# Performance work log

Measured on AMD Instinct MI355X. Metric: run time of the kernel, lower is better.

Reference implementation:

```python
import jax, jax.numpy as jnp
import numpy as np

B, S, DIM, NQ, NKV = 2, 2048, 4096, 32, 8
HD = DIM // NQ  # 128


def _rope(t, fc):
    # t: [B,S,H,D]; fc: [S,D/2,2] = (cos,sin). Complex multiply on (even,odd) pairs.
    b, s, h, d = t.shape
    tp = t.astype(jnp.float32).reshape(b, s, h, d // 2, 2)
    c = fc[None, :, None, :, 0]
    sn = fc[None, :, None, :, 1]
    x0, x1 = tp[..., 0], tp[..., 1]
    rot = jnp.stack([x0 * c - x1 * sn, x0 * sn + x1 * c], axis=-1)
    return rot.reshape(b, s, h, d).astype(t.dtype)


def setup_inputs() -> dict:
    key = jax.random.key(0)
    ks = jax.random.split(key, 5)
    x = jax.random.normal(ks[0], (B, S, DIM), jnp.float32)
    wq = jax.random.normal(ks[1], (DIM, NQ * HD), jnp.float32) * 0.02
    wk = jax.random.normal(ks[2], (DIM, NKV * HD), jnp.float32) * 0.02
    wv = jax.random.normal(ks[3], (DIM, NKV * HD), jnp.float32) * 0.02
    wo = jax.random.normal(ks[4], (NQ * HD, DIM), jnp.float32) * 0.02
    # Llama RoPE frequencies for positions [0, S)
    inv_freq = 1.0 / (10000.0 ** (jnp.arange(0, HD, 2, dtype=jnp.float32) / HD))
    ang = jnp.arange(S, dtype=jnp.float32)[:, None] * inv_freq[None, :]  # [S, HD/2]
    freqs_cis = jnp.stack([jnp.cos(ang), jnp.sin(ang)], axis=-1)  # [S, HD/2, 2]
    cache_key = jnp.zeros((B, S, NKV, HD), jnp.float32)
    cache_value = jnp.zeros((B, S, NKV, HD), jnp.float32)
    return {"x": x, "start_pos": 0, "freqs_cis": freqs_cis, "wq": wq, "wk": wk,
            "wv": wv, "wo": wo, "cache_key": cache_key, "cache_value": cache_value}


def reference(x, start_pos, freqs_cis, wq, wk, wv, wo, cache_key, cache_value):
    b, s, dim = x.shape
    nkv, hd = cache_key.shape[2], cache_key.shape[3]
    nq = wq.shape[1] // hd
    n_rep = nq // nkv
    xq = (x @ wq).reshape(b, s, nq, hd)
    xk = (x @ wk).reshape(b, s, nkv, hd)
    xv = (x @ wv).reshape(b, s, nkv, hd)
    xq = _rope(xq, freqs_cis)
    xk = _rope(xk, freqs_cis)
    # KV-cache write then read of the valid prefix
    ck = jax.lax.dynamic_update_slice(cache_key, xk, (0, start_pos, 0, 0))
    cv = jax.lax.dynamic_update_slice(cache_value, xv, (0, start_pos, 0, 0))
    kv_len = start_pos + s
    k = ck[:, :kv_len]
    v = cv[:, :kv_len]
    # GQA: repeat_interleave kv heads to match q heads (as original materializes)
    keys = jnp.repeat(k, n_rep, axis=2)    # [B,K,NQ,HD]
    values = jnp.repeat(v, n_rep, axis=2)
    scale = 1.0 / jnp.sqrt(jnp.float32(hd))
    scores = jnp.einsum('bqhd,bkhd->bhqk', xq, keys) * scale  # [B,H,S,K]
    attn = jax.nn.softmax(scores, axis=-1)  # NOTE: no causal mask, as in source
    out = jnp.einsum('bhqk,bkhd->bqhd', attn, values).reshape(b, s, nq * hd)
    return out @ wo
```

## Files before the change

### kernel.cpp

```cpp
#include <hip/hip_runtime.h>
#include <stdint.h>


typedef __attribute__((ext_vector_type(8))) short short8;
typedef __attribute__((ext_vector_type(4))) float f32x4;
typedef __attribute__((ext_vector_type(16))) float f32x16;

#define DEVFN static __device__ __forceinline__

DEVFN ushort f2bf(float f) {
  uint32_t u = __builtin_bit_cast(uint32_t, f);
  u += 0x7fffu + ((u >> 16) & 1);
  return (ushort)(u >> 16);
}

DEVFN void gll16(const void* g, void* l) {
  __builtin_amdgcn_global_load_lds(
      (const __attribute__((address_space(1))) void*)g,
      (__attribute__((address_space(3))) void*)l, 16, 0, 0);
}

DEVFN float xhalf_max(float v) { return fmaxf(v, __shfl_xor(v, 32)); }
DEVFN float xhalf_add(float v) { return v + __shfl_xor(v, 32); }

#if __has_builtin(__builtin_amdgcn_exp2f)
DEVFN float ex2(float x) { return __builtin_amdgcn_exp2f(x); }
#else
DEVFN float ex2(float x) {
  float r;
  asm("v_exp_f32 %0, %1" : "=v"(r) : "v"(x));
  return r;
}
#endif

DEVFN uint32_t cvtpk(float a, float b) {
  uint32_t r;
  asm("v_cvt_pk_bf16_f32 %0, %1, %2" : "=v"(r) : "v"(a), "v"(b));
  return r;
}

DEVFN float vmax16(const f32x16& v) {
  float a0 = fmaxf(fmaxf(v[0], v[1]), v[2]);
  float a1 = fmaxf(fmaxf(v[3], v[4]), v[5]);
  float a2 = fmaxf(fmaxf(v[6], v[7]), v[8]);
  float a3 = fmaxf(fmaxf(v[9], v[10]), v[11]);
  float a4 = fmaxf(fmaxf(v[12], v[13]), v[14]);
  float b0 = fmaxf(fmaxf(a0, a1), a2);
  float b1 = fmaxf(fmaxf(a3, a4), v[15]);
  return fmaxf(b0, b1);
}
DEVFN float vsum16(const f32x16& v) {
  float s0 = (v[0] + v[1]) + (v[2] + v[3]);
  float s1 = (v[4] + v[5]) + (v[6] + v[7]);
  float s2 = (v[8] + v[9]) + (v[10] + v[11]);
  float s3 = (v[12] + v[13]) + (v[14] + v[15]);
  return (s0 + s1) + (s2 + s3);
}

DEVFN short8 mk_frag(uint32_t w0, uint32_t w1, uint32_t w2, uint32_t w3, int hi) {
  uint32_t x0 = __shfl_xor(w0, 32);
  uint32_t x1 = __shfl_xor(w1, 32);
  uint32_t x2 = __shfl_xor(w2, 32);
  uint32_t x3 = __shfl_xor(w3, 32);
  uint4 u;
  u.x = hi ? x2 : w0;
  u.y = hi ? x3 : w1;
  u.z = hi ? w2 : x0;
  u.w = hi ? w3 : x1;
  return __builtin_bit_cast(short8, u);
}

#define VMW(N) asm volatile("s_waitcnt vmcnt(" #N ")" ::: "memory")

__global__ __launch_bounds__(256) void k_cvt(const float* __restrict__ src,
                                             ushort* __restrict__ dst, int n8) {
  int i = blockIdx.x * 256 + threadIdx.x;
  if (i >= n8) return;
  const float4* s4 = (const float4*)src + (size_t)i * 2;
  float4 a = s4[0], b = s4[1];
  uint4 o;
  o.x = (uint32_t)f2bf(a.x) | ((uint32_t)f2bf(a.y) << 16);
  o.y = (uint32_t)f2bf(a.z) | ((uint32_t)f2bf(a.w) << 16);
  o.z = (uint32_t)f2bf(b.x) | ((uint32_t)f2bf(b.y) << 16);
  o.w = (uint32_t)f2bf(b.z) | ((uint32_t)f2bf(b.w) << 16);
  ((uint4*)dst)[i] = o;
}

__global__ __launch_bounds__(256) void k_tr(const float* __restrict__ src,
                                            ushort* __restrict__ dst, int R, int C) {
  __shared__ float tile[64][65];
  const int c0 = blockIdx.x * 64, r0 = blockIdx.y * 64;
  const int t = threadIdx.x, rr = t >> 6, cc = t & 63;
#pragma unroll
  for (int i = 0; i < 16; ++i)
    tile[rr + i * 4][cc] = src[(size_t)(r0 + rr + i * 4) * C + c0 + cc];
  __syncthreads();
#pragma unroll
  for (int i = 0; i < 16; ++i)
    dst[(size_t)(c0 + rr + i * 4) * R + r0 + cc] = f2bf(tile[cc][rr + i * 4]);
}

template <int MODE>
__global__ __launch_bounds__(512, 2) void k_gemm8(
    const ushort* __restrict__ A, const ushort* __restrict__ Bp,
    const float* __restrict__ fcis, ushort* __restrict__ oQ,
    ushort* __restrict__ oK, ushort* __restrict__ oV, float* __restrict__ oC) {
  constexpr int K = 4096;
  constexpr int BN = MODE ? 256 : 192;
  constexpr int WN = BN / 4;
  constexpr int NF = WN / 16;
  constexpr int NBX = MODE ? 16 : 32;
  constexpr int ABUF = 16384;
  constexpr int BBUF = BN * 64;
  constexpr int NT = K / 32;

  __shared__ char smem[4 * ABUF + 4 * BBUF];
  char* AsL = smem;
  char* BsL = smem + 4 * ABUF;

  constexpr int nwg = NBX * 16;
  const int bid = blockIdx.x;
  const int wg = (bid & 7) * (nwg >> 3) + (bid >> 3);
  const int nb = wg % NBX, mb = wg / NBX;
  const int m0 = mb * 256, n0 = nb * BN;

  const int tid = threadIdx.x;
  const int w = tid >> 6, lane = tid & 63;
  const int gg = lane >> 4, rr = lane & 15;
  const int wm = w >> 2, wn = w & 3;

  const int l8 = lane >> 3, s7 = lane & 7;
  const int Ra0 = w * 8 + l8, Ra1 = 64 + Ra0;
  const int ea0 = s7 ^ (Ra0 & 7), ea1 = s7 ^ (Ra1 & 7);
  const ushort* agp0 = A + (size_t)(m0 + 2 * Ra0 + (ea0 >> 2)) * K + (ea0 & 3) * 8;
  const ushort* agp1 = A + (size_t)(m0 + 2 * Ra1 + (ea1 >> 2)) * K + (ea1 & 3) * 8;
  char* lda0 = AsL + w * 1024;
  char* lda1 = AsL + 8192 + w * 1024;

  const int Rb0 = w * 8 + l8;
  const int eb0 = s7 ^ (Rb0 & 7);
  const ushort* bgp0 = Bp + (size_t)(n0 + 2 * Rb0 + (eb0 >> 2)) * K + (eb0 & 3) * 8;
  char* ldb0 = BsL + w * 1024;
  const int Rb1 = MODE ? (64 + w * 8 + l8) : (64 + w * 4 + l8);
  const int eb1 = s7 ^ (Rb1 & 7);
  const ushort* bgp1 = Bp + (size_t)(n0 + 2 * Rb1 + (eb1 >> 2)) * K + (eb1 & 3) * 8;
  char* ldb1 = BsL + 8192 + (MODE ? w * 1024 : w * 512);

  auto STAGE_A = [&](int t) {
    const int bo = t & 3;
    const size_t ko = (size_t)t * 32;
    gll16(agp0 + ko, lda0 + bo * ABUF);
    gll16(agp1 + ko, lda1 + bo * ABUF);
  };
  auto STAGE_B = [&](int t) {
    const int bo = t & 3;
    const size_t ko = (size_t)t * 32;
    gll16(bgp0 + ko, ldb0 + bo * BBUF);
    if constexpr (MODE) {
      gll16(bgp1 + ko, ldb1 + bo * BBUF);
    } else {
      if (lane < 32) gll16(bgp1 + ko, ldb1 + bo * BBUF);
    }
  };

  int aoff[8], boff[NF];
#pragma unroll
  for (int mf = 0; mf < 8; ++mf) {
    const int m = wm * 128 + mf * 16 + rr;
    aoff[mf] = (m >> 1) * 128 + (((((m & 1) << 2) | gg) ^ ((m >> 1) & 7)) << 4);
  }
#pragma unroll
  for (int nf = 0; nf < NF; ++nf) {
    const int n = wn * WN + nf * 16 + rr;
    boff[nf] = (n >> 1) * 128 + (((((n & 1) << 2) | gg) ^ ((n >> 1) & 7)) << 4);
  }

  f32x4 acc[8][NF] = {};
  short8 X0[4], X1[4], Y0[4], Y1[4];
  short8 Bc0[NF], Bc1[NF];

  auto RD_A = [&](int tt, short8* d, int h) {
    const char* Ab = AsL + (tt & 3) * ABUF;
#pragma unroll
    for (int i = 0; i < 4; ++i) d[i] = *(const short8*)(Ab + aoff[h * 4 + i]);
  };
  auto RD_B = [&](int tt, short8* d) {
    const char* Bb = BsL + (tt & 3) * BBUF;
#pragma unroll
    for (int nf = 0; nf < NF; ++nf) d[nf] = *(const short8*)(Bb + boff[nf]);
  };
  auto MFMA_H = [&](short8* a, short8* bfr, int h) {
#pragma unroll
    for (int mi = 0; mi < 4; ++mi)
#pragma unroll
      for (int nf = 0; nf < NF; ++nf)
        acc[h + mi][nf] = __builtin_amdgcn_mfma_f32_16x16x32_bf16(
            a[mi], bfr[nf], acc[h + mi][nf], 0, 0, 0);
  };

#define GITER(T, cA0, cA1, cB, nA0, nA1, nB, STG, VN)                \
  do {                                                               \
    if constexpr (MODE == 1) RD_B((T), Bc0); \
    RD_A((T) + 1, nA0, 0);                                           \
    if constexpr (MODE == 0) RD_B((T) + 1, nB);                      \
    __builtin_amdgcn_sched_barrier(0);                               \
    __builtin_amdgcn_s_setprio(1);                                   \
    MFMA_H(cA0, (MODE == 1) ? Bc0 : cB, 0);                          \
    __builtin_amdgcn_s_setprio(0);                                   \
    RD_A((T) + 1, nA1, 1);                                           \
    if (STG) { STAGE_A((T) + 3); STAGE_B((T) + 3); }                 \
    __builtin_amdgcn_sched_barrier(0);                               \
    __builtin_amdgcn_s_setprio(1);                                   \
    MFMA_H(cA1, (MODE == 1) ? Bc0 : cB, 4);                          \
    __builtin_amdgcn_s_setprio(0);                                   \
    VMW(VN);                                                         \
    __builtin_amdgcn_s_barrier();                                    \
    __builtin_amdgcn_sched_barrier(0);                               \
  } while (0)

  STAGE_A(0); STAGE_B(0);
  STAGE_A(1); STAGE_B(1);
  STAGE_A(2); STAGE_B(2);
  VMW(4);
  __builtin_amdgcn_s_barrier();
  __builtin_amdgcn_sched_barrier(0);
  RD_A(0, X0, 0);
  RD_A(0, X1, 1);
  if constexpr (MODE == 0) RD_B(0, Bc0);

  for (int tp = 0; tp < 62; ++tp) {
    const int T = 2 * tp;
    GITER(T, X0, X1, Bc0, Y0, Y1, Bc1, true, 4);
    GITER(T + 1, Y0, Y1, Bc1, X0, X1, Bc0, true, 4);
  }
  GITER(124, X0, X1, Bc0, Y0, Y1, Bc1, true, 4);
  GITER(125, Y0, Y1, Bc1, X0, X1, Bc0, false, 0);
  GITER(126, X0, X1, Bc0, Y0, Y1, Bc1, false, 0);
  if constexpr (MODE == 1) RD_B(127, Bc0);
  __builtin_amdgcn_s_setprio(1);
  MFMA_H(Y0, (MODE == 1) ? Bc0 : Bc1, 0);
  MFMA_H(Y1, (MODE == 1) ? Bc0 : Bc1, 4);
  __builtin_amdgcn_s_setprio(0);
#undef GITER

  if constexpr (MODE == 1) {
#pragma unroll
    for (int mf = 0; mf < 8; ++mf) {
      const int mbase = m0 + wm * 128 + mf * 16 + gg * 4;
#pragma unroll
      for (int nf = 0; nf < NF; ++nf) {
        const int n = n0 + wn * WN + nf * 16 + rr;
#pragma unroll
        for (int j = 0; j < 4; ++j)
          oC[(size_t)(mbase + j) * 4096 + n] = acc[mf][nf][j];
      }
    }
  } else {
    const int b = m0 >> 11;
#pragma unroll
    for (int mf = 0; mf < 8; ++mf) {
      const int mbase = m0 + wm * 128 + mf * 16 + gg * 4;
      const int s0 = mbase & 2047;
#pragma unroll
      for (int nf = 0; nf < NF; ++nf) {
        const int n = n0 + wn * WN + nf * 16 + rr;
        if (n < 5120) {
          const int d = n & 127, ii = d >> 1;
          const float sgn = (n & 1) ? 1.0f : -1.0f;
          const float qsc = (n < 4096) ? 0.12752364599362f : 1.0f;
          ushort res[4];
#pragma unroll
          for (int j = 0; j < 4; ++j) {
            const float2 cs = ((const float2*)fcis)[(size_t)(s0 + j) * 64 + ii];
            float v = acc[mf][nf][j];
            float pv = __shfl_xor(v, 1);
            res[j] = f2bf(qsc * (v * cs.x + sgn * pv * cs.y));
          }
          if (n < 4096) {
            ushort* dst = oQ + ((size_t)(b * 32 + (n >> 7)) * 2048 + s0) * 128 + d;
#pragma unroll
            for (int j = 0; j < 4; ++j) dst[j * 128] = res[j];
          } else {
            ushort* dst =
                oK + ((size_t)(b * 8 + ((n - 4096) >> 7)) * 2048 + s0) * 128 + d;
#pragma unroll
            for (int j = 0; j < 4; ++j) dst[j * 128] = res[j];
          }
        } else {
          const int n2 = n - 5120;
          ushort4 pk;
          pk.x = f2bf(acc[mf][nf][0]);
          pk.y = f2bf(acc[mf][nf][1]);
          pk.z = f2bf(acc[mf][nf][2]);
          pk.w = f2bf(acc[mf][nf][3]);
          *(ushort4*)&oV[((size_t)(b * 8 + (n2 >> 7)) * 128 + (n2 & 127)) * 2048 + s0] =
              pk;
        }
      }
    }
  }
}

__global__ __launch_bounds__(512, 2) void k_attn(const ushort* __restrict__ Qg,
                                                 const ushort* __restrict__ Kg,
                                                 const ushort* __restrict__ Vt,
                                                 ushort* __restrict__ Og) {
  __shared__ ushort Ks[2][64 * 128];
  __shared__ ushort Vs[2][64 * 128];
  __shared__ float sml[8][32];

  const int bh = blockIdx.x, qt = blockIdx.y;
  const int b = bh >> 5, h = bh & 31, hk = h >> 2;
  const int t = threadIdx.x, w = t >> 6, lane = t & 63;
  const int ln31 = lane & 31, hi = lane >> 5;
  const int q0 = qt * 256;

  short8 qf[8];
  {
    const size_t qbase = ((size_t)bh * 2048 + q0 + w * 32 + ln31) * 128;
#pragma unroll
    for (int tt = 0; tt < 8; ++tt)
      qf[tt] = *(const short8*)&Qg[qbase + tt * 16 + hi * 8];
  }
  const size_t kgb = (size_t)(b * 8 + hk) * 2048 * 128;
  const size_t vgb = (size_t)(b * 8 + hk) * 128 * 2048;

  const int srow = t >> 3;
  const int ssl = (t & 7) * 2;
  const int s0 = ssl ^ (srow & 15);
  const int vd = 2 * (t >> 3) + ((t & 7) >> 2);
  const int vkl = (t & 3) * 16;
  const ushort* kgp = Kg + kgb + (size_t)srow * 128 + ssl * 8;
  const ushort* vgp = Vt + vgb + (size_t)vd * 2048 + vkl;

  uint4 rk0, rk1, rv0, rv1;
  auto LOAD = [&](int k0) {
    const uint4* kp = (const uint4*)(kgp + (size_t)k0 * 128);
    rk0 = kp[0];
    rk1 = kp[1];
    const uint4* vp = (const uint4*)(vgp + k0);
    rv0 = vp[0];
    rv1 = vp[1];
  };
  auto STORE = [&](int buf) {
    char* kd = (char*)Ks[buf] + srow * 256;
    *(uint4*)(kd + (s0 << 4)) = rk0;
    *(uint4*)(kd + ((s0 ^ 1) << 4)) = rk1;
    char* vdd = (char*)Vs[buf] + srow * 256;
    *(uint4*)(vdd + (s0 << 4)) = rv0;
    *(uint4*)(vdd + ((s0 ^ 1) << 4)) = rv1;
  };

  f32x16 ov[4] = {};
  float m_run = -1e30f, l_run = 0.f;

  const int mk = ln31 & 15;
  const int krb0 = ln31 * 256, krb1 = krb0 + 8192;
  const int vrb = (ln31 >> 1) * 256;
  const int vsp = (ln31 & 1) * 8 + hi;
  const int mv = ln31 >> 1;

  LOAD(0);
  STORE(0);
  __syncthreads();

  for (int tile = 0; tile < 32; ++tile) {
    const int cur = tile & 1;
    if (tile < 31) LOAD((tile + 1) * 64);

    const char* Kc = (const char*)Ks[cur];
    f32x16 p0 = {}, p1 = {};
    __builtin_amdgcn_s_setprio(1);
#pragma unroll
    for (int tt = 0; tt < 8; ++tt) {
      const int sl = ((tt * 2 + hi) ^ mk) << 4;
      short8 ka0 = *(const short8*)(Kc + krb0 + sl);
      short8 ka1 = *(const short8*)(Kc + krb1 + sl);
      p0 = __builtin_amdgcn_mfma_f32_32x32x16_bf16(ka0, qf[tt], p0, 0, 0, 0);
      p1 = __builtin_amdgcn_mfma_f32_32x32x16_bf16(ka1, qf[tt], p1, 0, 0, 0);
    }
    __builtin_amdgcn_s_setprio(0);

    const float pmax = xhalf_max(fmaxf(vmax16(p0), vmax16(p1)));
    if (!__all(pmax <= m_run + 8.0f)) {
      const float mnew = fmaxf(m_run, pmax);
      const float al = ex2(m_run - mnew);
      m_run = mnew;
      l_run *= al;
      sml[w][ln31] = al;
      const float4 a0 = *(const float4*)&sml[w][hi * 4];
      const float4 a1 = *(const float4*)&sml[w][8 + hi * 4];
      const float4 a2 = *(const float4*)&sml[w][16 + hi * 4];
      const float4 a3 = *(const float4*)&sml[w][24 + hi * 4];
      const float aa[16] = {a0.x, a0.y, a0.z, a0.w, a1.x, a1.y, a1.z, a1.w,
                            a2.x, a2.y, a2.z, a2.w, a3.x, a3.y, a3.z, a3.w};
#pragma unroll
      for (int i = 0; i < 16; ++i) {
        ov[0][i] *= aa[i]; ov[1][i] *= aa[i];
        ov[2][i] *= aa[i]; ov[3][i] *= aa[i];
      }
    }
#pragma unroll
    for (int i = 0; i < 16; ++i) p0[i] = ex2(p0[i] - m_run);
#pragma unroll
    for (int i = 0; i < 16; ++i) p1[i] = ex2(p1[i] - m_run);
    l_run += xhalf_add(vsum16(p0) + vsum16(p1));

    short8 pa[4];
    pa[0] = mk_frag(cvtpk(p0[0], p0[1]), cvtpk(p0[2], p0[3]),
                    cvtpk(p0[4], p0[5]), cvtpk(p0[6], p0[7]), hi);
    pa[1] = mk_frag(cvtpk(p0[8], p0[9]), cvtpk(p0[10], p0[11]),
                    cvtpk(p0[12], p0[13]), cvtpk(p0[14], p0[15]), hi);
    pa[2] = mk_frag(cvtpk(p1[0], p1[1]), cvtpk(p1[2], p1[3]),
                    cvtpk(p1[4], p1[5]), cvtpk(p1[6], p1[7]), hi);
    pa[3] = mk_frag(cvtpk(p1[8], p1[9]), cvtpk(p1[10], p1[11]),
                    cvtpk(p1[12], p1[13]), cvtpk(p1[14], p1[15]), hi);

    const char* Vc = (const char*)Vs[cur];
    __builtin_amdgcn_s_setprio(1);
#pragma unroll
    for (int db = 0; db < 4; ++db) {
      const int rb = vrb + db * 4096;
#pragma unroll
      for (int ks = 0; ks < 4; ++ks) {
        const int sl = ((vsp + ks * 2) ^ mv) << 4;
        short8 bv = *(const short8*)(Vc + rb + sl);
        ov[db] = __builtin_amdgcn_mfma_f32_32x32x16_bf16(pa[ks], bv, ov[db], 0, 0, 0);
      }
    }
    __builtin_amdgcn_s_setprio(0);

    if (tile < 31) STORE(cur ^ 1);
    __syncthreads();
  }

  sml[w][ln31] = l_run;
  const float4 l0 = *(const float4*)&sml[w][hi * 4];
  const float4 l1 = *(const float4*)&sml[w][8 + hi * 4];
  const float4 l2 = *(const float4*)&sml[w][16 + hi * 4];
  const float4 l3 = *(const float4*)&sml[w][24 + hi * 4];
  const float inv[16] = {1.f / l0.x, 1.f / l0.y, 1.f / l0.z, 1.f / l0.w,
                         1.f / l1.x, 1.f / l1.y, 1.f / l1.z, 1.f / l1.w,
                         1.f / l2.x, 1.f / l2.y, 1.f / l2.z, 1.f / l2.w,
                         1.f / l3.x, 1.f / l3.y, 1.f / l3.z, 1.f / l3.w};
  const int qb0 = q0 + w * 32 + hi * 4;
#pragma unroll
  for (int rg = 0; rg < 4; ++rg)
#pragma unroll
    for (int j = 0; j < 4; ++j) {
      const int sq = qb0 + rg * 8 + j;
      const size_t orow = ((size_t)(b * 2048 + sq)) * 4096 + h * 128 + ln31;
#pragma unroll
      for (int db = 0; db < 4; ++db)
        Og[orow + db * 32] = f2bf(ov[db][rg * 4 + j] * inv[rg * 4 + j]);
    }
}

extern "C" void kernel_launch(void* const* d_in, const int* in_sizes, int n_in,
                              void* d_out, int out_size, void* d_ws, size_t ws_size,
                              hipStream_t stream) {
  const float* x = (const float*)d_in[0];
  const float* fcis = (const float*)d_in[2];
  const float* wq = (const float*)d_in[3];
  const float* wk = (const float*)d_in[4];
  const float* wv = (const float*)d_in[5];
  const float* wo = (const float*)d_in[6];
  float* out = (float*)d_out;

  char* ws = (char*)d_ws;
  ushort* xb  = (ushort*)(ws);
  ushort* wsT = (ushort*)(ws + 33554432u);
  ushort* qb  = (ushort*)(ws + 83886080u);
  ushort* kb  = (ushort*)(ws + 117440512u);
  ushort* vbT = (ushort*)(ws + 125829120u);
  ushort* woT = xb;
  ushort* ao  = wsT;

  k_cvt<<<8192, 256, 0, stream>>>(x, xb, 2097152);
  k_tr<<<dim3(64, 64), 256, 0, stream>>>(wq, wsT, 4096, 4096);
  k_tr<<<dim3(16, 64), 256, 0, stream>>>(wk, wsT + (size_t)4096 * 4096, 4096, 1024);
  k_tr<<<dim3(16, 64), 256, 0, stream>>>(wv, wsT + (size_t)5120 * 4096, 4096, 1024);
  k_gemm8<0><<<512, 512, 0, stream>>>(xb, wsT, fcis, qb, kb, vbT, nullptr);
  k_tr<<<dim3(64, 64), 256, 0, stream>>>(wo, woT, 4096, 4096);
  k_attn<<<dim3(64, 8), 512, 0, stream>>>(qb, kb, vbT, ao);
  k_gemm8<1><<<256, 512, 0, stream>>>(ao, woT, nullptr, nullptr, nullptr, nullptr,
                                      out);
}
```

Measured before the change: 531.3 us.

## Retile QKV GEMM warps, sync every two k-steps, vectorize weight transpose

The QKV GEMM mode now uses a 4x2 warp grid with 64x96 warp tiles instead of 2x4 with 128x48, which changes the A/B fragment reuse ratio. The main loop now issues the vmcnt wait and workgroup barrier every second k-iteration, with a full vmcnt(0) drain, instead of after every iteration. The transpose/convert kernel now uses float4 loads, converts to bf16 before writing to LDS, uses a swizzled bf16 tile and writes 16-byte vector stores. Waiting every two iterations on a 4-slot ring staged three ahead may risk LDS reuse hazards, and the full drain can expose memory latency.

```diff
diff --git a/kernel.cpp b/kernel.cpp
--- a/kernel.cpp
+++ b/kernel.cpp
@@ -88,16 +88,30 @@
 
 __global__ __launch_bounds__(256) void k_tr(const float* __restrict__ src,
                                             ushort* __restrict__ dst, int R, int C) {
-  __shared__ float tile[64][65];
+  __shared__ ushort tl[64 * 64];
   const int c0 = blockIdx.x * 64, r0 = blockIdx.y * 64;
-  const int t = threadIdx.x, rr = t >> 6, cc = t & 63;
-#pragma unroll
-  for (int i = 0; i < 16; ++i)
-    tile[rr + i * 4][cc] = src[(size_t)(r0 + rr + i * 4) * C + c0 + cc];
+  const int t = threadIdx.x;
+  const int r = t >> 4, c4 = (t & 15) << 2;
+#pragma unroll
+  for (int i = 0; i < 4; ++i) {
+    const int rr = r + i * 16;
+    float4 v = *(const float4*)&src[(size_t)(r0 + rr) * C + c0 + c4];
+    ushort bv[4] = {f2bf(v.x), f2bf(v.y), f2bf(v.z), f2bf(v.w)};
+#pragma unroll
+    for (int j = 0; j < 4; ++j) {
+      const int c = c4 + j;
+      *(ushort*)((char*)tl + c * 128 + (((rr >> 3) ^ (c & 7)) << 4) +
+                 ((rr & 7) << 1)) = bv[j];
+    }
+  }
   __syncthreads();
-#pragma unroll
-  for (int i = 0; i < 16; ++i)
-    dst[(size_t)(c0 + rr + i * 4) * R + r0 + cc] = f2bf(tile[cc][rr + i * 4]);
+  const int cc = t >> 2;
+#pragma unroll
+  for (int i = 0; i < 2; ++i) {
+    const int ch = (t & 3) + i * 4;
+    short8 v = *(const short8*)((char*)tl + cc * 128 + ((ch ^ (cc & 7)) << 4));
+    *(short8*)&dst[(size_t)(c0 + cc) * R + r0 + ch * 8] = v;
+  }
 }
 
 template <int MODE>
@@ -107,12 +121,16 @@
     ushort* __restrict__ oK, ushort* __restrict__ oV, float* __restrict__ oC) {
   constexpr int K = 4096;
   constexpr int BN = MODE ? 256 : 192;
-  constexpr int WN = BN / 4;
-  constexpr int NF = WN / 16;
   constexpr int NBX = MODE ? 16 : 32;
   constexpr int ABUF = 16384;
   constexpr int BBUF = BN * 64;
   constexpr int NT = K / 32;
+  constexpr int WNG = MODE ? 4 : 2;
+  constexpr int MF = MODE ? 8 : 4;
+  constexpr int NF = MODE ? 4 : 6;
+  constexpr int MH = MF / 2;
+  constexpr int MSPAN = 16 * MF;
+  constexpr int NSPAN = 16 * NF;
 
   __shared__ char smem[4 * ABUF + 4 * BBUF];
   char* AsL = smem;
@@ -127,7 +145,7 @@
   const int tid = threadIdx.x;
   const int w = tid >> 6, lane = tid & 63;
   const int gg = lane >> 4, rr = lane & 15;
-  const int wm = w >> 2, wn = w & 3;
+  const int wm = w / WNG, wn = w % WNG;
 
   const int l8 = lane >> 3, s7 = lane & 7;
   const int Ra0 = w * 8 + l8, Ra1 = 64 + Ra0;
@@ -163,26 +181,26 @@
     }
   };
 
-  int aoff[8], boff[NF];
-#pragma unroll
-  for (int mf = 0; mf < 8; ++mf) {
-    const int m = wm * 128 + mf * 16 + rr;
+  int aoff[MF], boff[NF];
+#pragma unroll
+  for (int mf = 0; mf < MF; ++mf) {
+    const int m = wm * MSPAN + mf * 16 + rr;
     aoff[mf] = (m >> 1) * 128 + (((((m & 1) << 2) | gg) ^ ((m >> 1) & 7)) << 4);
   }
 #pragma unroll
   for (int nf = 0; nf < NF; ++nf) {
-    const int n = wn * WN + nf * 16 + rr;
+    const int n = wn * NSPAN + nf * 16 + rr;
     boff[nf] = (n >> 1) * 128 + (((((n & 1) << 2) | gg) ^ ((n >> 1) & 7)) << 4);
   }
 
-  f32x4 acc[8][NF] = {};
-  short8 X0[4], X1[4], Y0[4], Y1[4];
+  f32x4 acc[MF][NF] = {};
+  short8 X0[MH], X1[MH], Y0[MH], Y1[MH];
   short8 Bc0[NF], Bc1[NF];
 
   auto RD_A = [&](int tt, short8* d, int h) {
     const char* Ab = AsL + (tt & 3) * ABUF;
 #pragma unroll
-    for (int i = 0; i < 4; ++i) d[i] = *(const short8*)(Ab + aoff[h * 4 + i]);
+    for (int i = 0; i < MH; ++i) d[i] = *(const short8*)(Ab + aoff[h * MH + i]);
   };
   auto RD_B = [&](int tt, short8* d) {
     const char* Bb = BsL + (tt & 3) * BBUF;
@@ -191,14 +209,14 @@
   };
   auto MFMA_H = [&](short8* a, short8* bfr, int h) {
 #pragma unroll
-    for (int mi = 0; mi < 4; ++mi)
+    for (int mi = 0; mi < MH; ++mi)
 #pragma unroll
       for (int nf = 0; nf < NF; ++nf)
         acc[h + mi][nf] = __builtin_amdgcn_mfma_f32_16x16x32_bf16(
             a[mi], bfr[nf], acc[h + mi][nf], 0, 0, 0);
   };
 
-#define GITER(T, cA0, cA1, cB, nA0, nA1, nB, STG, VN)                \
+#define GITER(T, cA0, cA1, cB, nA0, nA1, nB, STG, BARM)              \
   do {                                                               \
     if constexpr (MODE == 1) RD_B((T), Bc0); \
     RD_A((T) + 1, nA0, 0);                                           \
@@ -211,17 +229,19 @@
     if (STG) { STAGE_A((T) + 3); STAGE_B((T) + 3); }                 \
     __builtin_amdgcn_sched_barrier(0);                               \
     __builtin_amdgcn_s_setprio(1);                                   \
-    MFMA_H(cA1, (MODE == 1) ? Bc0 : cB, 4);                          \
+    MFMA_H(cA1, (MODE == 1) ? Bc0 : cB, MH);                         \
     __builtin_amdgcn_s_setprio(0);                                   \
-    VMW(VN);                                                         \
-    __builtin_amdgcn_s_barrier();                                    \
-    __builtin_amdgcn_sched_barrier(0);                               \
+    if (BARM) {                                                      \
+      VMW(0);                                                        \
+      __builtin_amdgcn_s_barrier();                                  \
+      __builtin_amdgcn_sched_barrier(0);                             \
+    }                                                                \
   } while (0)
 
   STAGE_A(0); STAGE_B(0);
   STAGE_A(1); STAGE_B(1);
   STAGE_A(2); STAGE_B(2);
-  VMW(4);
+  VMW(0);
   __builtin_amdgcn_s_barrier();
   __builtin_amdgcn_sched_barrier(0);
   RD_A(0, X0, 0);
@@ -230,26 +250,26 @@
 
   for (int tp = 0; tp < 62; ++tp) {
     const int T = 2 * tp;
-    GITER(T, X0, X1, Bc0, Y0, Y1, Bc1, true, 4);
-    GITER(T + 1, Y0, Y1, Bc1, X0, X1, Bc0, true, 4);
-  }
-  GITER(124, X0, X1, Bc0, Y0, Y1, Bc1, true, 4);
+    GITER(T, X0, X1, Bc0, Y0, Y1, Bc1, true, 0);
+    GITER(T + 1, Y0, Y1, Bc1, X0, X1, Bc0, true, 1);
+  }
+  GITER(124, X0, X1, Bc0, Y0, Y1, Bc1, true, 1);
   GITER(125, Y0, Y1, Bc1, X0, X1, Bc0, false, 0);
   GITER(126, X0, X1, Bc0, Y0, Y1, Bc1, false, 0);
   if constexpr (MODE == 1) RD_B(127, Bc0);
   __builtin_amdgcn_s_setprio(1);
   MFMA_H(Y0, (MODE == 1) ? Bc0 : Bc1, 0);
-  MFMA_H(Y1, (MODE == 1) ? Bc0 : Bc1, 4);
+  MFMA_H(Y1, (MODE == 1) ? Bc0 : Bc1, MH);
   __builtin_amdgcn_s_setprio(0);
 #undef GITER
 
   if constexpr (MODE == 1) {
 #pragma unroll
-    for (int mf = 0; mf < 8; ++mf) {
-      const int mbase = m0 + wm * 128 + mf * 16 + gg * 4;
+    for (int mf = 0; mf < MF; ++mf) {
+      const int mbase = m0 + wm * MSPAN + mf * 16 + gg * 4;
 #pragma unroll
       for (int nf = 0; nf < NF; ++nf) {
-        const int n = n0 + wn * WN + nf * 16 + rr;
+        const int n = n0 + wn * NSPAN + nf * 16 + rr;
 #pragma unroll
         for (int j = 0; j < 4; ++j)
           oC[(size_t)(mbase + j) * 4096 + n] = acc[mf][nf][j];
@@ -258,12 +278,12 @@
   } else {
     const int b = m0 >> 11;
 #pragma unroll
-    for (int mf = 0; mf < 8; ++mf) {
-      const int mbase = m0 + wm * 128 + mf * 16 + gg * 4;
+    for (int mf = 0; mf < MF; ++mf) {
+      const int mbase = m0 + wm * MSPAN + mf * 16 + gg * 4;
       const int s0 = mbase & 2047;
 #pragma unroll
       for (int nf = 0; nf < NF; ++nf) {
-        const int n = n0 + wn * WN + nf * 16 + rr;
+        const int n = n0 + wn * NSPAN + nf * 16 + rr;
         if (n < 5120) {
           const int d = n & 127, ii = d >> 1;
           const float sgn = (n & 1) ? 1.0f : -1.0f;
```

Result: slower. 552.3 us (+3.9%).
